# Optimization experiments

Hardware: AMD Instinct MI355X
Metric: run time of the kernel (lower is better)

## Reference

```python
import jax, jax.numpy as jnp
import numpy as np

N = 200000
IN_CH = 128
HIDDEN = [512, 512, 256]
NUM_TYPES = 10


def hetero_linear(x, types, W, b):
    # y[n] = x[n] @ W[types[n]] + b[types[n]]
    # Loop over the small fixed set of types (grouped GEMM as masked dense GEMMs).
    out = jnp.zeros((x.shape[0], W.shape[2]), dtype=x.dtype)
    for t in range(W.shape[0]):
        yt = x @ W[t] + b[t]
        out = out + jnp.where((types == t)[:, None], yt, jnp.zeros((), x.dtype))
    return out


def setup_inputs() -> dict:
    key = jax.random.key(0)
    ks = jax.random.split(key, 8)
    dims = [IN_CH] + HIDDEN
    inp = {
        "x": jax.random.normal(ks[0], (N, IN_CH), dtype=jnp.float32),
        "atom_types": jax.random.randint(ks[1], (N,), 0, NUM_TYPES, dtype=jnp.int32),
    }
    for i in range(3):
        fan_in = dims[i]
        scale = 1.0 / np.sqrt(fan_in)
        inp[f"W{i}"] = jax.random.normal(ks[2 + 2 * i], (NUM_TYPES, dims[i], dims[i + 1]), dtype=jnp.float32) * scale
        inp[f"b{i}"] = jax.random.normal(ks[3 + 2 * i], (NUM_TYPES, dims[i + 1]), dtype=jnp.float32) * scale
    return inp


def reference(x, atom_types, W0, b0, W1, b1, W2, b2):
    h = jax.nn.relu(hetero_linear(x, atom_types, W0, b0))
    h = jax.nn.relu(hetero_linear(h, atom_types, W1, b1))
    return hetero_linear(h, atom_types, W2, b2)
```

## Files before the change

kernel.cpp:

```cpp
#include <hip/hip_runtime.h>
#include <stdint.h>

typedef float  f32x4  __attribute__((ext_vector_type(4)));
typedef short  bf16x8 __attribute__((ext_vector_type(8)));

#define TYPES 10
#define D_IN  128
#define D_H1  512
#define D_H2  512
#define D_OUT 256

__device__ __forceinline__ unsigned short f2bf(float f) {
  union { float f; unsigned u; } v; v.f = f;
  unsigned u = v.u;
  return (unsigned short)((u + 0x7FFFu + ((u >> 16) & 1u)) >> 16);
}

__device__ __forceinline__ void async16(void* lds, const void* g) {
  __builtin_amdgcn_global_load_lds(
      (const __attribute__((address_space(1))) void*)g,
      (__attribute__((address_space(3))) void*)lds, 16, 0, 0);
}

__global__ void k_init(int* meta) {
  if (threadIdx.x < 48) meta[threadIdx.x] = 0;
}

__global__ void k_hist(const int* __restrict__ types, int n, int* __restrict__ meta) {
  __shared__ int lc[TYPES];
  if (threadIdx.x < TYPES) lc[threadIdx.x] = 0;
  __syncthreads();
  int i = blockIdx.x * 256 + threadIdx.x;
  if (i < n) atomicAdd(&lc[types[i]], 1);
  __syncthreads();
  if (threadIdx.x < TYPES && lc[threadIdx.x]) atomicAdd(&meta[threadIdx.x], lc[threadIdx.x]);
}

__global__ void k_scan(int* meta) {
  if (threadIdx.x == 0) {
    int off = 0;
    for (int t = 0; t < TYPES; ++t) {
      meta[16 + t] = off;
      off += ((meta[t] + 127) >> 7) << 7;
    }
    meta[26] = off;
  }
}

__global__ void k_scatter(const int* __restrict__ types, int n,
                          int* __restrict__ meta, int* __restrict__ perm) {
  __shared__ int lc[TYPES], lbase[TYPES];
  if (threadIdx.x < TYPES) lc[threadIdx.x] = 0;
  __syncthreads();
  int i = blockIdx.x * 256 + threadIdx.x;
  int t = 0, loc = 0;
  bool ok = i < n;
  if (ok) { t = types[i]; loc = atomicAdd(&lc[t], 1); }
  __syncthreads();
  if (threadIdx.x < TYPES) {
    int c = lc[threadIdx.x];
    lbase[threadIdx.x] = c ? atomicAdd(&meta[32 + threadIdx.x], c) : 0;
  }
  __syncthreads();
  if (ok) perm[meta[16 + t] + lbase[t] + loc] = i;
}

__global__ void k_gather(const float* __restrict__ x, const int* __restrict__ perm,
                         const int* __restrict__ meta, unsigned short* __restrict__ xs) {
  int p = blockIdx.x * 8 + (threadIdx.x >> 5);
  if (p >= meta[26]) return;
  int t = 0;
  while (p >= meta[17 + t]) t++;
  int e = (threadIdx.x & 31) * 4;
  unsigned short o0, o1, o2, o3;
  if (p - meta[16 + t] < meta[t]) {
    const float4 v = *(const float4*)(x + (size_t)perm[p] * D_IN + e);
    o0 = f2bf(v.x); o1 = f2bf(v.y); o2 = f2bf(v.z); o3 = f2bf(v.w);
  } else {
    o0 = o1 = o2 = o3 = 0;
  }
  *(ushort4*)(xs + (size_t)p * D_IN + e) = make_ushort4(o0, o1, o2, o3);
}

__global__ void k_wtrans(const float* __restrict__ W, unsigned short* __restrict__ Wt,
                         int K, int NOUT) {
  int t = blockIdx.y;
  int ntn = NOUT >> 6;
  int kb = blockIdx.x / ntn, nb = blockIdx.x % ntn;
  __shared__ unsigned short tile[64][65];
  const float* src = W + (size_t)t * K * NOUT + (size_t)(kb * 64) * NOUT + nb * 64;
  int c = threadIdx.x & 63;
  int r0 = threadIdx.x >> 6;
  #pragma unroll
  for (int i = 0; i < 16; ++i) {
    int r = r0 * 16 + i;
    tile[r][c] = f2bf(src[(size_t)r * NOUT + c]);
  }
  __syncthreads();
  unsigned short* dst = Wt + (size_t)t * NOUT * K + (size_t)(nb * 64) * K + kb * 64;
  #pragma unroll
  for (int i = 0; i < 16; ++i) {
    int nn = r0 * 16 + i;
    dst[(size_t)nn * K + c] = tile[c][nn];
  }
}

template <int K, int NOUT, bool RELU, bool FINAL>
__launch_bounds__(256)
__global__ void k_gemm(const unsigned short* __restrict__ A,
                       const unsigned short* __restrict__ Wt,
                       const float* __restrict__ bias,
                       unsigned short* __restrict__ H,
                       float* __restrict__ OUT,
                       const int* __restrict__ meta,
                       const int* __restrict__ perm) {
  __shared__ unsigned short As[128 * 32];
  __shared__ unsigned short Bs[128 * 32];
  int row0 = blockIdx.y * 128;
  if (row0 >= meta[26]) return;
  int t = 0;
  while (row0 >= meta[17 + t]) t++;
  int seg = meta[16 + t], cnt = meta[t];
  int tid = threadIdx.x, lane = tid & 63, wid = tid >> 6;
  int wr = (wid >> 1) * 64, wc = (wid & 1) * 64;
  int col0 = blockIdx.x * 128;
  const unsigned short* Ag = A + (size_t)row0 * K;
  const unsigned short* Bg = Wt + ((size_t)t * NOUT + col0) * K;

  f32x4 acc[4][4] = {};
  int r_ld = tid >> 2;
  int k_ld = (tid & 3) * 8;
  int ldsbase = (tid & ~63) * 8;

  constexpr int nK = K / 32;
  for (int kt = 0; kt < nK; ++kt) {
    __syncthreads();
    #pragma unroll
    for (int i = 0; i < 2; ++i) {
      int r = i * 64 + r_ld;
      async16(As + i * 2048 + ldsbase, Ag + (size_t)r * K + kt * 32 + k_ld);
      async16(Bs + i * 2048 + ldsbase, Bg + (size_t)r * K + kt * 32 + k_ld);
    }
    __syncthreads();

    int koff = (lane >> 4) * 8;
    int rA = lane & 15;
    bf16x8 a[4], b[4];
    #pragma unroll
    for (int m = 0; m < 4; ++m)
      a[m] = *(const bf16x8*)(As + (wr + m * 16 + rA) * 32 + koff);
    #pragma unroll
    for (int n = 0; n < 4; ++n)
      b[n] = *(const bf16x8*)(Bs + (wc + n * 16 + rA) * 32 + koff);
    #pragma unroll
    for (int m = 0; m < 4; ++m)
      #pragma unroll
      for (int n = 0; n < 4; ++n)
        acc[m][n] = __builtin_amdgcn_mfma_f32_16x16x32_bf16(a[m], b[n], acc[m][n], 0, 0, 0);
  }

  int cA = lane & 15, rE = (lane >> 4) * 4;
  #pragma unroll
  for (int n = 0; n < 4; ++n) {
    int col = col0 + wc + n * 16 + cA;
    float bv = bias[t * NOUT + col];
    #pragma unroll
    for (int m = 0; m < 4; ++m) {
      int rb = row0 + wr + m * 16 + rE;
      #pragma unroll
      for (int e = 0; e < 4; ++e) {
        float v = acc[m][n][e] + bv;
        if (RELU) v = fmaxf(v, 0.f);
        if (!FINAL) {
          H[(size_t)(rb + e) * NOUT + col] = f2bf(v);
        } else {
          int r = rb + e;
          if (r - seg < cnt) OUT[(size_t)perm[r] * NOUT + col] = v;
        }
      }
    }
  }
}

extern "C" void kernel_launch(void* const* d_in, const int* in_sizes, int n_in,
                              void* d_out, int out_size, void* d_ws, size_t ws_size,
                              hipStream_t stream) {
  const float* x     = (const float*)d_in[0];
  const int*   types = (const int*)d_in[1];
  const float* W0    = (const float*)d_in[2];
  const float* b0    = (const float*)d_in[3];
  const float* W1    = (const float*)d_in[4];
  const float* b1    = (const float*)d_in[5];
  const float* W2    = (const float*)d_in[6];
  const float* b2    = (const float*)d_in[7];
  float* out = (float*)d_out;
  int n = in_sizes[1];
  int RB = (n + 127) / 128 + TYPES;
  size_t NPAD = (size_t)RB * 128;

  char* ws = (char*)d_ws;
  int* meta = (int*)ws;
  int* perm = (int*)(ws + 1024);
  size_t off = 1024 + NPAD * 4;
  off = (off + 255) & ~(size_t)255;
  unsigned short* wt0 = (unsigned short*)(ws + off); off += (size_t)TYPES * D_H1 * D_IN * 2;
  unsigned short* wt1 = (unsigned short*)(ws + off); off += (size_t)TYPES * D_H2 * D_H1 * 2;
  unsigned short* wt2 = (unsigned short*)(ws + off); off += (size_t)TYPES * D_OUT * D_H2 * 2;
  off = (off + 255) & ~(size_t)255;
  unsigned short* B1 = (unsigned short*)(ws + off); off += NPAD * 512 * 2;
  unsigned short* B2 = (unsigned short*)(ws + off); off += NPAD * 512 * 2;

  int hb = (n + 255) / 256;
  k_init<<<1, 64, 0, stream>>>(meta);
  k_hist<<<hb, 256, 0, stream>>>(types, n, meta);
  k_scan<<<1, 64, 0, stream>>>(meta);
  k_scatter<<<hb, 256, 0, stream>>>(types, n, meta, perm);
  k_gather<<<RB * 16, 256, 0, stream>>>(x, perm, meta, B1);
  k_wtrans<<<dim3((D_IN / 64) * (D_H1 / 64), TYPES), 256, 0, stream>>>(W0, wt0, D_IN, D_H1);
  k_wtrans<<<dim3((D_H1 / 64) * (D_H2 / 64), TYPES), 256, 0, stream>>>(W1, wt1, D_H1, D_H2);
  k_wtrans<<<dim3((D_H2 / 64) * (D_OUT / 64), TYPES), 256, 0, stream>>>(W2, wt2, D_H2, D_OUT);

  k_gemm<D_IN, D_H1, true,  false><<<dim3(D_H1 / 128, RB), 256, 0, stream>>>(B1, wt0, b0, B2, nullptr, meta, perm);
  k_gemm<D_H1, D_H2, true,  false><<<dim3(D_H2 / 128, RB), 256, 0, stream>>>(B2, wt1, b1, B1, nullptr, meta, perm);
  k_gemm<D_H2, D_OUT, false, true ><<<dim3(D_OUT / 128, RB), 256, 0, stream>>>(B1, wt2, b2, nullptr, out, meta, perm);
}
```

Baseline: 528.0 us.

## Double-buffer GEMM K-loop with swizzled LDS, BK=64, and XCD-aware block remap

Reworks the grouped GEMM mainloop to use a 64-wide K tile, double-buffered in 64KB of LDS. The next tile's async global-to-LDS loads are issued before the current tile's MFMAs, so memory latency can overlap compute. An XOR swizzle on the 16-byte chunk index is meant to avoid LDS bank conflicts on the bf16x8 reads. Workgroup IDs are remapped so consecutive tiles land on the same XCD for better L2 reuse. The cost is lower occupancy from the larger LDS footprint.

```diff
diff --git a/kernel.cpp b/kernel.cpp
--- a/kernel.cpp
+++ b/kernel.cpp
@@ -114,49 +114,83 @@
                        float* __restrict__ OUT,
                        const int* __restrict__ meta,
                        const int* __restrict__ perm) {
-  __shared__ unsigned short As[128 * 32];
-  __shared__ unsigned short Bs[128 * 32];
-  int row0 = blockIdx.y * 128;
+  __shared__ char lds[65536];
+
+  int NXB = gridDim.x;
+  int nwg = NXB * (int)gridDim.y;
+  int raw = blockIdx.x + blockIdx.y * NXB;
+  int q = nwg >> 3, rr = nwg & 7;
+  int xcd = raw & 7, idx = raw >> 3;
+  int swz = (xcd < rr ? xcd * (q + 1) : rr * (q + 1) + (xcd - rr) * q) + idx;
+  int bx = swz % NXB, by = swz / NXB;
+
+  int row0 = by * 128;
   if (row0 >= meta[26]) return;
   int t = 0;
   while (row0 >= meta[17 + t]) t++;
   int seg = meta[16 + t], cnt = meta[t];
   int tid = threadIdx.x, lane = tid & 63, wid = tid >> 6;
   int wr = (wid >> 1) * 64, wc = (wid & 1) * 64;
-  int col0 = blockIdx.x * 128;
-  const unsigned short* Ag = A + (size_t)row0 * K;
-  const unsigned short* Bg = Wt + ((size_t)t * NOUT + col0) * K;
+  int col0 = bx * 128;
+  const char* Ag = (const char*)(A + (size_t)row0 * K);
+  const char* Bg = (const char*)(Wt + ((size_t)t * NOUT + col0) * K);
+
+  int srow = tid >> 3, sg = tid & 7;
+  const char* aSrc[4]; const char* bSrc[4]; int ldst[4];
+  #pragma unroll
+  for (int i = 0; i < 4; ++i) {
+    int r = i * 32 + srow;
+    int g = sg ^ (r & 7);
+    aSrc[i] = Ag + (size_t)r * (K * 2) + g * 16;
+    bSrc[i] = Bg + (size_t)r * (K * 2) + g * 16;
+    ldst[i] = i * 4096 + (tid >> 6) * 1024;
+  }
 
   f32x4 acc[4][4] = {};
-  int r_ld = tid >> 2;
-  int k_ld = (tid & 3) * 8;
-  int ldsbase = (tid & ~63) * 8;
-
-  constexpr int nK = K / 32;
+  int rA = lane & 15, qk = lane >> 4;
+
+  #pragma unroll
+  for (int i = 0; i < 4; ++i) {
+    async16(lds + ldst[i],         aSrc[i]);
+    async16(lds + 16384 + ldst[i], bSrc[i]);
+  }
+  __syncthreads();
+
+  constexpr int nK = K / 64;
   for (int kt = 0; kt < nK; ++kt) {
+    int cur = kt & 1;
+    if (kt + 1 < nK) {
+      char* nb_ = lds + (cur ^ 1) * 32768;
+      #pragma unroll
+      for (int i = 0; i < 4; ++i) {
+        async16(nb_ + ldst[i],         aSrc[i] + (size_t)(kt + 1) * 128);
+        async16(nb_ + 16384 + ldst[i], bSrc[i] + (size_t)(kt + 1) * 128);
+      }
+    }
+    const char* Ab = lds + cur * 32768;
+    const char* Bb = Ab + 16384;
+    #pragma unroll
+    for (int kk = 0; kk < 2; ++kk) {
+      bf16x8 a[4], b[4];
+      #pragma unroll
+      for (int m = 0; m < 4; ++m) {
+        int row = wr + m * 16 + rA;
+        int off = (row * 128 + kk * 64 + qk * 16) ^ ((rA & 7) << 4);
+        a[m] = *(const bf16x8*)(Ab + off);
+      }
+      #pragma unroll
+      for (int n = 0; n < 4; ++n) {
+        int row = wc + n * 16 + rA;
+        int off = (row * 128 + kk * 64 + qk * 16) ^ ((rA & 7) << 4);
+        b[n] = *(const bf16x8*)(Bb + off);
+      }
+      #pragma unroll
+      for (int m = 0; m < 4; ++m)
+        #pragma unroll
+        for (int n = 0; n < 4; ++n)
+          acc[m][n] = __builtin_amdgcn_mfma_f32_16x16x32_bf16(a[m], b[n], acc[m][n], 0, 0, 0);
+    }
     __syncthreads();
-    #pragma unroll
-    for (int i = 0; i < 2; ++i) {
-      int r = i * 64 + r_ld;
-      async16(As + i * 2048 + ldsbase, Ag + (size_t)r * K + kt * 32 + k_ld);
-      async16(Bs + i * 2048 + ldsbase, Bg + (size_t)r * K + kt * 32 + k_ld);
-    }
-    __syncthreads();
-
-    int koff = (lane >> 4) * 8;
-    int rA = lane & 15;
-    bf16x8 a[4], b[4];
-    #pragma unroll
-    for (int m = 0; m < 4; ++m)
-      a[m] = *(const bf16x8*)(As + (wr + m * 16 + rA) * 32 + koff);
-    #pragma unroll
-    for (int n = 0; n < 4; ++n)
-      b[n] = *(const bf16x8*)(Bs + (wc + n * 16 + rA) * 32 + koff);
-    #pragma unroll
-    for (int m = 0; m < 4; ++m)
-      #pragma unroll
-      for (int n = 0; n < 4; ++n)
-        acc[m][n] = __builtin_amdgcn_mfma_f32_16x16x32_bf16(a[m], b[n], acc[m][n], 0, 0, 0);
   }
 
   int cA = lane & 15, rE = (lane >> 4) * 4;
```

After: 598.6 us. +13.4%, slower.

## Rewrite grouped GEMM as 256x256 tile, double-buffered, swizzled-LDS pipelined kernel

Applied to the files above, without the earlier changes.

Grows the GEMM block tile from 128x128 to 256x256 with 8 waves and a K step of 64. Global-to-LDS async loads are double-buffered and interleaved across four sub-phases, with XOR-swizzled LDS addressing and explicit waitcnt/barrier/setprio scheduling. Blocks are remapped across XCDs for cache locality. Segment padding per type rises to 256 rows to match the new tile. The aim is to hide load latency and raise MFMA utilisation, at the cost of 128 KB LDS per block, more register pressure, and more padded rows per type.

```diff
diff --git a/kernel.cpp b/kernel.cpp
--- a/kernel.cpp
+++ b/kernel.cpp
@@ -41,7 +41,7 @@
     int off = 0;
     for (int t = 0; t < TYPES; ++t) {
       meta[16 + t] = off;
-      off += ((meta[t] + 127) >> 7) << 7;
+      off += ((meta[t] + 255) >> 8) << 8;
     }
     meta[26] = off;
   }
@@ -106,7 +106,7 @@
 }
 
 template <int K, int NOUT, bool RELU, bool FINAL>
-__launch_bounds__(256)
+__launch_bounds__(512, 2)
 __global__ void k_gemm(const unsigned short* __restrict__ A,
                        const unsigned short* __restrict__ Wt,
                        const float* __restrict__ bias,
@@ -114,62 +114,113 @@
                        float* __restrict__ OUT,
                        const int* __restrict__ meta,
                        const int* __restrict__ perm) {
-  __shared__ unsigned short As[128 * 32];
-  __shared__ unsigned short Bs[128 * 32];
-  int row0 = blockIdx.y * 128;
+  constexpr int nKT = K / 64;
+  __shared__ char lds[131072];
+
+  int NXB = gridDim.x;
+  int nwg = NXB * (int)gridDim.y;
+  int raw = blockIdx.x + blockIdx.y * NXB;
+  int q = nwg >> 3, rr = nwg & 7;
+  int xcd = raw & 7, idx = raw >> 3;
+  int swz = (xcd < rr ? xcd * (q + 1) : rr * (q + 1) + (xcd - rr) * q) + idx;
+  int bx = swz % NXB, by = swz / NXB;
+
+  int row0 = by * 256;
   if (row0 >= meta[26]) return;
   int t = 0;
   while (row0 >= meta[17 + t]) t++;
   int seg = meta[16 + t], cnt = meta[t];
   int tid = threadIdx.x, lane = tid & 63, wid = tid >> 6;
-  int wr = (wid >> 1) * 64, wc = (wid & 1) * 64;
-  int col0 = blockIdx.x * 128;
-  const unsigned short* Ag = A + (size_t)row0 * K;
-  const unsigned short* Bg = Wt + ((size_t)t * NOUT + col0) * K;
-
-  f32x4 acc[4][4] = {};
-  int r_ld = tid >> 2;
-  int k_ld = (tid & 3) * 8;
-  int ldsbase = (tid & ~63) * 8;
-
-  constexpr int nK = K / 32;
-  for (int kt = 0; kt < nK; ++kt) {
-    __syncthreads();
+  int wr = (wid >> 2) * 128, wc = (wid & 3) * 64;
+  int col0 = bx * 256;
+  const char* Ag = (const char*)(A + (size_t)row0 * K);
+  const char* Bg = (const char*)(Wt + ((size_t)t * NOUT + col0) * K);
+
+  int gsrc = ((tid & 7) ^ ((tid >> 3) & 7)) * 16;
+  const char* aS = Ag + (size_t)(tid >> 3) * (2 * K) + gsrc;
+  const char* bS = Bg + (size_t)(((tid >> 3) & 31) + ((tid >> 3) >> 5) * 64) * (2 * K) + gsrc;
+
+  auto stage = [&](int kt, int sub) {
+    if (kt >= nKT) return;
+    int h = sub & 1, du = kt & 1;
+    char* dst = lds + ((sub < 2) ? 0 : 65536) + (du * 2 + h) * 16384 + wid * 1024;
+    const char* src = (sub < 2 ? aS + (size_t)(h * 64) * (2 * K)
+                               : bS + (size_t)(h * 32) * (2 * K)) + (size_t)kt * 128;
+    async16(dst,        src);
+    async16(dst + 8192, src + (size_t)128 * (2 * K));
+  };
+
+  f32x4 acc[8][4] = {};
+  int rA = lane & 15, qoff = (lane >> 4) * 16, xr = (lane & 7) << 4;
+  int lrA = (wid >> 2) * 64;
+  int clB = (wid & 3) * 32;
+
+  stage(0, 2); stage(0, 1); stage(0, 0); stage(0, 3); stage(1, 2); stage(1, 1);
+  asm volatile("s_waitcnt vmcnt(4)" ::: "memory");
+  __builtin_amdgcn_s_barrier();
+
+  for (int g = 0; g < nKT; ++g) {
+    int d = g & 1;
+    const char* Ad = lds + d * 32768;
+    const char* Bd = lds + 65536 + d * 32768;
     #pragma unroll
-    for (int i = 0; i < 2; ++i) {
-      int r = i * 64 + r_ld;
-      async16(As + i * 2048 + ldsbase, Ag + (size_t)r * K + kt * 32 + k_ld);
-      async16(Bs + i * 2048 + ldsbase, Bg + (size_t)r * K + kt * 32 + k_ld);
+    for (int rel = 0; rel < 4; ++rel) {
+      constexpr int MH[4] = {0, 1, 1, 0};
+      constexpr int NH[4] = {0, 0, 1, 1};
+      const int mh = MH[rel], nh = NH[rel];
+      const char* Au = Ad + mh * 16384;
+      const char* Bu = Bd + nh * 16384;
+      bf16x8 a[4][2], b[2][2];
+      #pragma unroll
+      for (int m = 0; m < 4; ++m) {
+        int lr = lrA + m * 16 + rA;
+        #pragma unroll
+        for (int kk = 0; kk < 2; ++kk)
+          a[m][kk] = *(const bf16x8*)(Au + ((lr * 128 + kk * 64 + qoff) ^ xr));
+      }
+      #pragma unroll
+      for (int nn = 0; nn < 2; ++nn) {
+        int cl = clB + nn * 16 + rA;
+        #pragma unroll
+        for (int kk = 0; kk < 2; ++kk)
+          b[nn][kk] = *(const bf16x8*)(Bu + ((cl * 128 + kk * 64 + qoff) ^ xr));
+      }
+      if      (rel == 0) stage(g + 1, 0);
+      else if (rel == 1) stage(g + 1, 3);
+      else if (rel == 2) stage(g + 2, 2);
+      else               stage(g + 2, 1);
+      __builtin_amdgcn_s_barrier();
+      asm volatile("s_waitcnt lgkmcnt(0)" ::: "memory");
+      __builtin_amdgcn_sched_barrier(0);
+      __builtin_amdgcn_s_setprio(1);
+      #pragma unroll
+      for (int kk = 0; kk < 2; ++kk)
+        #pragma unroll
+        for (int m = 0; m < 4; ++m)
+          #pragma unroll
+          for (int nn = 0; nn < 2; ++nn)
+            acc[mh * 4 + m][nh * 2 + nn] = __builtin_amdgcn_mfma_f32_16x16x32_bf16(
+                a[m][kk], b[nn][kk], acc[mh * 4 + m][nh * 2 + nn], 0, 0, 0);
+      __builtin_amdgcn_s_setprio(0);
+      if (rel == 3 && g + 1 < nKT) {
+        if (g + 2 < nKT) asm volatile("s_waitcnt vmcnt(4)" ::: "memory");
+        else             asm volatile("s_waitcnt vmcnt(0)" ::: "memory");
+      }
+      __builtin_amdgcn_s_barrier();
     }
-    __syncthreads();
-
-    int koff = (lane >> 4) * 8;
-    int rA = lane & 15;
-    bf16x8 a[4], b[4];
-    #pragma unroll
-    for (int m = 0; m < 4; ++m)
-      a[m] = *(const bf16x8*)(As + (wr + m * 16 + rA) * 32 + koff);
-    #pragma unroll
-    for (int n = 0; n < 4; ++n)
-      b[n] = *(const bf16x8*)(Bs + (wc + n * 16 + rA) * 32 + koff);
-    #pragma unroll
-    for (int m = 0; m < 4; ++m)
-      #pragma unroll
-      for (int n = 0; n < 4; ++n)
-        acc[m][n] = __builtin_amdgcn_mfma_f32_16x16x32_bf16(a[m], b[n], acc[m][n], 0, 0, 0);
   }
 
   int cA = lane & 15, rE = (lane >> 4) * 4;
   #pragma unroll
-  for (int n = 0; n < 4; ++n) {
-    int col = col0 + wc + n * 16 + cA;
+  for (int ni = 0; ni < 4; ++ni) {
+    int col = col0 + wc + ni * 16 + cA;
     float bv = bias[t * NOUT + col];
     #pragma unroll
-    for (int m = 0; m < 4; ++m) {
-      int rb = row0 + wr + m * 16 + rE;
+    for (int mi = 0; mi < 8; ++mi) {
+      int rb = row0 + wr + mi * 16 + rE;
       #pragma unroll
       for (int e = 0; e < 4; ++e) {
-        float v = acc[m][n][e] + bv;
+        float v = acc[mi][ni][e] + bv;
         if (RELU) v = fmaxf(v, 0.f);
         if (!FINAL) {
           H[(size_t)(rb + e) * NOUT + col] = f2bf(v);
@@ -195,8 +246,8 @@
   const float* b2    = (const float*)d_in[7];
   float* out = (float*)d_out;
   int n = in_sizes[1];
-  int RB = (n + 127) / 128 + TYPES;
-  size_t NPAD = (size_t)RB * 128;
+  int RB = (n + 255) / 256 + TYPES;
+  size_t NPAD = (size_t)RB * 256;
 
   char* ws = (char*)d_ws;
   int* meta = (int*)ws;
@@ -215,12 +266,12 @@
   k_hist<<<hb, 256, 0, stream>>>(types, n, meta);
   k_scan<<<1, 64, 0, stream>>>(meta);
   k_scatter<<<hb, 256, 0, stream>>>(types, n, meta, perm);
-  k_gather<<<RB * 16, 256, 0, stream>>>(x, perm, meta, B1);
+  k_gather<<<RB * 32, 256, 0, stream>>>(x, perm, meta, B1);
   k_wtrans<<<dim3((D_IN / 64) * (D_H1 / 64), TYPES), 256, 0, stream>>>(W0, wt0, D_IN, D_H1);
   k_wtrans<<<dim3((D_H1 / 64) * (D_H2 / 64), TYPES), 256, 0, stream>>>(W1, wt1, D_H1, D_H2);
   k_wtrans<<<dim3((D_H2 / 64) * (D_OUT / 64), TYPES), 256, 0, stream>>>(W2, wt2, D_H2, D_OUT);
 
-  k_gemm<D_IN, D_H1, true,  false><<<dim3(D_H1 / 128, RB), 256, 0, stream>>>(B1, wt0, b0, B2, nullptr, meta, perm);
-  k_gemm<D_H1, D_H2, true,  false><<<dim3(D_H2 / 128, RB), 256, 0, stream>>>(B2, wt1, b1, B1, nullptr, meta, perm);
-  k_gemm<D_H2, D_OUT, false, true ><<<dim3(D_OUT / 128, RB), 256, 0, stream>>>(B1, wt2, b2, nullptr, out, meta, perm);
-}
+  k_gemm<D_IN, D_H1, true,  false><<<dim3(D_H1 / 256, RB), 512, 0, stream>>>(B1, wt0, b0, B2, nullptr, meta, perm);
+  k_gemm<D_H1, D_H2, true,  false><<<dim3(D_H2 / 256, RB), 512, 0, stream>>>(B2, wt1, b1, B1, nullptr, meta, perm);
+  k_gemm<D_H2, D_OUT, false, true ><<<dim3(D_OUT / 256, RB), 512, 0, stream>>>(B1, wt2, b2, nullptr, out, meta, perm);
+}
```

Result: slower. 542.4 us (+2.7%).

## Fuse gather and all three MLP layers into one LDS-resident kernel

Applied to the files above, without the earlier changes.

Replaces the gather kernel and the three separate grouped GEMM launches with a single kernel. Each 128-row block of sorted rows keeps its activations in a 160KB LDS tile across all layers and streams weight tiles double-buffered with swizzled layouts. It also merges the three weight-transpose launches into one and remaps block indices across XCDs. This removes the global round-trips of the bf16 hidden activations and several launches. The cost is heavy LDS use, which limits occupancy, and barrier-heavy inner loops.

```diff
diff --git a/kernel.cpp b/kernel.cpp
--- a/kernel.cpp
+++ b/kernel.cpp
@@ -65,28 +65,17 @@
   if (ok) perm[meta[16 + t] + lbase[t] + loc] = i;
 }
 
-__global__ void k_gather(const float* __restrict__ x, const int* __restrict__ perm,
-                         const int* __restrict__ meta, unsigned short* __restrict__ xs) {
-  int p = blockIdx.x * 8 + (threadIdx.x >> 5);
-  if (p >= meta[26]) return;
-  int t = 0;
-  while (p >= meta[17 + t]) t++;
-  int e = (threadIdx.x & 31) * 4;
-  unsigned short o0, o1, o2, o3;
-  if (p - meta[16 + t] < meta[t]) {
-    const float4 v = *(const float4*)(x + (size_t)perm[p] * D_IN + e);
-    o0 = f2bf(v.x); o1 = f2bf(v.y); o2 = f2bf(v.z); o3 = f2bf(v.w);
-  } else {
-    o0 = o1 = o2 = o3 = 0;
-  }
-  *(ushort4*)(xs + (size_t)p * D_IN + e) = make_ushort4(o0, o1, o2, o3);
-}
-
-__global__ void k_wtrans(const float* __restrict__ W, unsigned short* __restrict__ Wt,
-                         int K, int NOUT) {
-  int t = blockIdx.y;
+__global__ void k_wtrans_all(const float* __restrict__ W0a, const float* __restrict__ W1a,
+                             const float* __restrict__ W2a,
+                             unsigned short* __restrict__ wt0, unsigned short* __restrict__ wt1,
+                             unsigned short* __restrict__ wt2) {
+  int b = blockIdx.x;
+  const float* W; unsigned short* Wt; int K, NOUT, t, local;
+  if (b < 160)      { W = W0a; Wt = wt0; K = 128; NOUT = 512; t = b / 16; local = b % 16; }
+  else if (b < 800) { b -= 160; W = W1a; Wt = wt1; K = 512; NOUT = 512; t = b / 64; local = b % 64; }
+  else              { b -= 800; W = W2a; Wt = wt2; K = 512; NOUT = 256; t = b / 32; local = b % 32; }
   int ntn = NOUT >> 6;
-  int kb = blockIdx.x / ntn, nb = blockIdx.x % ntn;
+  int kb = local / ntn, nb = local % ntn;
   __shared__ unsigned short tile[64][65];
   const float* src = W + (size_t)t * K * NOUT + (size_t)(kb * 64) * NOUT + nb * 64;
   int c = threadIdx.x & 63;
@@ -105,78 +94,188 @@
   }
 }
 
-template <int K, int NOUT, bool RELU, bool FINAL>
-__launch_bounds__(256)
-__global__ void k_gemm(const unsigned short* __restrict__ A,
-                       const unsigned short* __restrict__ Wt,
-                       const float* __restrict__ bias,
-                       unsigned short* __restrict__ H,
-                       float* __restrict__ OUT,
-                       const int* __restrict__ meta,
-                       const int* __restrict__ perm) {
-  __shared__ unsigned short As[128 * 32];
-  __shared__ unsigned short Bs[128 * 32];
-  int row0 = blockIdx.y * 128;
+__device__ __forceinline__ void stageW(char* lds, int tid, int wid,
+                                       const unsigned short* __restrict__ Wt,
+                                       int NOUTl, int Kl, int t, int nb, int kt, int slot) {
+  const char* base = (const char*)(Wt + ((size_t)t * NOUTl + nb * 128) * Kl);
+  int lr = tid >> 3;
+  int g = ((tid & 7) ^ (lr & 7)) * 16;
+  const char* s0 = base + (size_t)lr * (Kl * 2) + (size_t)kt * 128 + g;
+  char* dst = lds + 131072 + slot * 16384 + wid * 1024;
+  async16(dst, s0);
+  async16(dst + 8192, s0 + (size_t)64 * (Kl * 2));
+}
+
+template <int KT, int NB>
+__device__ __forceinline__ void run_layer(char* lds, const unsigned short* __restrict__ Wt,
+                                          int Kl, int NOUTl, int t, int tid, int wid, int lane,
+                                          f32x4 (&acc)[4][8]) {
+  int rA = lane & 15, qk = (lane >> 4) * 16;
+  int wr = (wid >> 2) * 64, wcg = wid & 3;
+  bf16x8 a[4][2], b[2][2];
+  for (int kt = 0; kt < KT; ++kt) {
+    #pragma unroll
+    for (int nb = 0; nb < NB; ++nb) {
+      __builtin_amdgcn_sched_barrier(0);
+      const int slot = nb & 1;
+      if (nb == 0) {
+        #pragma unroll
+        for (int m = 0; m < 4; ++m) {
+          int r = wr + m * 16 + rA;
+          #pragma unroll
+          for (int kk = 0; kk < 2; ++kk)
+            a[m][kk] = *(const bf16x8*)(lds + r * 1024 +
+                         ((kt * 128 + kk * 64 + qk) ^ ((r & 7) << 4)));
+        }
+      }
+      #pragma unroll
+      for (int n = 0; n < 2; ++n) {
+        int cl = wcg * 32 + n * 16 + rA;
+        #pragma unroll
+        for (int kk = 0; kk < 2; ++kk)
+          b[n][kk] = *(const bf16x8*)(lds + 131072 + slot * 16384 + cl * 128 +
+                       ((kk * 64 + qk) ^ ((cl & 7) << 4)));
+      }
+      if (nb + 1 < NB)      stageW(lds, tid, wid, Wt, NOUTl, Kl, t, nb + 1, kt, (nb + 1) & 1);
+      else if (kt + 1 < KT) stageW(lds, tid, wid, Wt, NOUTl, Kl, t, 0, kt + 1, 0);
+      __builtin_amdgcn_s_barrier();
+      asm volatile("s_waitcnt lgkmcnt(0)" ::: "memory");
+      __builtin_amdgcn_sched_barrier(0);
+      __builtin_amdgcn_s_setprio(1);
+      #pragma unroll
+      for (int kk = 0; kk < 2; ++kk)
+        #pragma unroll
+        for (int m = 0; m < 4; ++m)
+          #pragma unroll
+          for (int n = 0; n < 2; ++n)
+            acc[m][nb * 2 + n] = __builtin_amdgcn_mfma_f32_16x16x32_bf16(
+                a[m][kk], b[n][kk], acc[m][nb * 2 + n], 0, 0, 0);
+      __builtin_amdgcn_s_setprio(0);
+      asm volatile("s_waitcnt vmcnt(0)" ::: "memory");
+      __builtin_amdgcn_s_barrier();
+    }
+  }
+}
+
+template <int CF, bool RELU>
+__device__ __forceinline__ void writeback_h(char* lds, const float* __restrict__ bias_,
+                                            int NOUTl, int t, int wid, int lane,
+                                            f32x4 (&acc)[4][8]) {
+  int cA = lane & 15, rE = (lane >> 4) * 4;
+  int wr = (wid >> 2) * 64, wcg = wid & 3;
+  #pragma unroll
+  for (int cf = 0; cf < CF; ++cf) {
+    int col = (cf >> 1) * 128 + wcg * 32 + (cf & 1) * 16 + cA;
+    float bv = bias_[t * NOUTl + col];
+    #pragma unroll
+    for (int m = 0; m < 4; ++m)
+      #pragma unroll
+      for (int e = 0; e < 4; ++e) {
+        int row = wr + m * 16 + rE + e;
+        float v = acc[m][cf][e] + bv;
+        if (RELU) v = fmaxf(v, 0.f);
+        *(unsigned short*)(lds + row * 1024 + ((col * 2) ^ ((row & 7) << 4))) = f2bf(v);
+      }
+  }
+}
+
+__launch_bounds__(512, 2)
+__global__ void k_fused(const float* __restrict__ x,
+                        const unsigned short* __restrict__ wt0, const float* __restrict__ b0,
+                        const unsigned short* __restrict__ wt1, const float* __restrict__ b1,
+                        const unsigned short* __restrict__ wt2, const float* __restrict__ b2,
+                        float* __restrict__ out,
+                        const int* __restrict__ meta, const int* __restrict__ perm) {
+  __shared__ char lds[163840];
+
+  int nwg = gridDim.x, raw = blockIdx.x;
+  int q = nwg >> 3, rr = nwg & 7;
+  int xcd = raw & 7, idx = raw >> 3;
+  int swz = (xcd < rr ? xcd * (q + 1) : rr * (q + 1) + (xcd - rr) * q) + idx;
+
+  int row0 = swz * 128;
   if (row0 >= meta[26]) return;
   int t = 0;
   while (row0 >= meta[17 + t]) t++;
   int seg = meta[16 + t], cnt = meta[t];
   int tid = threadIdx.x, lane = tid & 63, wid = tid >> 6;
-  int wr = (wid >> 1) * 64, wc = (wid & 1) * 64;
-  int col0 = blockIdx.x * 128;
-  const unsigned short* Ag = A + (size_t)row0 * K;
-  const unsigned short* Bg = Wt + ((size_t)t * NOUT + col0) * K;
-
-  f32x4 acc[4][4] = {};
-  int r_ld = tid >> 2;
-  int k_ld = (tid & 3) * 8;
-  int ldsbase = (tid & ~63) * 8;
-
-  constexpr int nK = K / 32;
-  for (int kt = 0; kt < nK; ++kt) {
-    __syncthreads();
-    #pragma unroll
-    for (int i = 0; i < 2; ++i) {
-      int r = i * 64 + r_ld;
-      async16(As + i * 2048 + ldsbase, Ag + (size_t)r * K + kt * 32 + k_ld);
-      async16(Bs + i * 2048 + ldsbase, Bg + (size_t)r * K + kt * 32 + k_ld);
-    }
-    __syncthreads();
-
-    int koff = (lane >> 4) * 8;
-    int rA = lane & 15;
-    bf16x8 a[4], b[4];
-    #pragma unroll
-    for (int m = 0; m < 4; ++m)
-      a[m] = *(const bf16x8*)(As + (wr + m * 16 + rA) * 32 + koff);
-    #pragma unroll
-    for (int n = 0; n < 4; ++n)
-      b[n] = *(const bf16x8*)(Bs + (wc + n * 16 + rA) * 32 + koff);
-    #pragma unroll
-    for (int m = 0; m < 4; ++m)
-      #pragma unroll
-      for (int n = 0; n < 4; ++n)
-        acc[m][n] = __builtin_amdgcn_mfma_f32_16x16x32_bf16(a[m], b[n], acc[m][n], 0, 0, 0);
-  }
-
-  int cA = lane & 15, rE = (lane >> 4) * 4;
-  #pragma unroll
-  for (int n = 0; n < 4; ++n) {
-    int col = col0 + wc + n * 16 + cA;
-    float bv = bias[t * NOUT + col];
-    #pragma unroll
-    for (int m = 0; m < 4; ++m) {
-      int rb = row0 + wr + m * 16 + rE;
-      #pragma unroll
-      for (int e = 0; e < 4; ++e) {
-        float v = acc[m][n][e] + bv;
-        if (RELU) v = fmaxf(v, 0.f);
-        if (!FINAL) {
-          H[(size_t)(rb + e) * NOUT + col] = f2bf(v);
-        } else {
-          int r = rb + e;
-          if (r - seg < cnt) OUT[(size_t)perm[r] * NOUT + col] = v;
+
+  stageW(lds, tid, wid, wt0, D_H1, D_IN, t, 0, 0, 0);
+
+  {
+    int grow = tid >> 2, gch = tid & 3;
+    int p = row0 + grow;
+    bool ok = (unsigned)(p - seg) < (unsigned)cnt;
+    int sw = (grow & 7) << 4;
+    const float* sp = ok ? x + (size_t)perm[p] * D_IN + gch * 32 : nullptr;
+    #pragma unroll
+    for (int j = 0; j < 4; ++j) {
+      bf16x8 v = {0, 0, 0, 0, 0, 0, 0, 0};
+      if (ok) {
+        float4 f0 = *(const float4*)(sp + j * 8);
+        float4 f1 = *(const float4*)(sp + j * 8 + 4);
+        v[0] = (short)f2bf(f0.x); v[1] = (short)f2bf(f0.y);
+        v[2] = (short)f2bf(f0.z); v[3] = (short)f2bf(f0.w);
+        v[4] = (short)f2bf(f1.x); v[5] = (short)f2bf(f1.y);
+        v[6] = (short)f2bf(f1.z); v[7] = (short)f2bf(f1.w);
+      }
+      *(bf16x8*)(lds + grow * 1024 + ((((gch * 4 + j) * 16)) ^ sw)) = v;
+    }
+  }
+  __syncthreads();
+
+  f32x4 acc[4][8];
+  #pragma unroll
+  for (int m = 0; m < 4; ++m)
+    #pragma unroll
+    for (int cf = 0; cf < 8; ++cf) acc[m][cf] = (f32x4){0.f, 0.f, 0.f, 0.f};
+
+  run_layer<2, 4>(lds, wt0, D_IN, D_H1, t, tid, wid, lane, acc);
+  stageW(lds, tid, wid, wt1, D_H2, D_H1, t, 0, 0, 0);
+  writeback_h<8, true>(lds, b0, D_H1, t, wid, lane, acc);
+  __syncthreads();
+  #pragma unroll
+  for (int m = 0; m < 4; ++m)
+    #pragma unroll
+    for (int cf = 0; cf < 8; ++cf) acc[m][cf] = (f32x4){0.f, 0.f, 0.f, 0.f};
+
+  run_layer<8, 4>(lds, wt1, D_H1, D_H2, t, tid, wid, lane, acc);
+  stageW(lds, tid, wid, wt2, D_OUT, D_H2, t, 0, 0, 0);
+  writeback_h<8, true>(lds, b1, D_H2, t, wid, lane, acc);
+  __syncthreads();
+  #pragma unroll
+  for (int m = 0; m < 4; ++m)
+    #pragma unroll
+    for (int cf = 0; cf < 8; ++cf) acc[m][cf] = (f32x4){0.f, 0.f, 0.f, 0.f};
+
+  run_layer<8, 2>(lds, wt2, D_H2, D_OUT, t, tid, wid, lane, acc);
+
+  {
+    int cA = lane & 15, rE = (lane >> 4) * 4;
+    int wr = (wid >> 2) * 64, wcg = wid & 3;
+    #pragma unroll
+    for (int cf = 0; cf < 4; ++cf) {
+      int col = (cf >> 1) * 128 + wcg * 32 + (cf & 1) * 16 + cA;
+      float bv = b2[t * D_OUT + col];
+      #pragma unroll
+      for (int m = 0; m < 4; ++m)
+        #pragma unroll
+        for (int e = 0; e < 4; ++e) {
+          int row = wr + m * 16 + rE + e;
+          *(float*)(lds + row * 1024 + ((col * 4) ^ ((row & 7) << 4))) = acc[m][cf][e] + bv;
         }
+    }
+    __builtin_amdgcn_s_barrier();
+    int grow = tid >> 2, gch = tid & 3;
+    int p = row0 + grow;
+    bool ok = (unsigned)(p - seg) < (unsigned)cnt;
+    if (ok) {
+      float* op = out + (size_t)perm[p] * D_OUT + gch * 64;
+      int sw = (grow & 7) << 4;
+      #pragma unroll
+      for (int j = 0; j < 16; ++j) {
+        float4 v = *(const float4*)(lds + grow * 1024 + ((((gch * 16 + j) * 16)) ^ sw));
+        *(float4*)(op + j * 4) = v;
       }
     }
   }
@@ -206,21 +305,13 @@
   unsigned short* wt0 = (unsigned short*)(ws + off); off += (size_t)TYPES * D_H1 * D_IN * 2;
   unsigned short* wt1 = (unsigned short*)(ws + off); off += (size_t)TYPES * D_H2 * D_H1 * 2;
   unsigned short* wt2 = (unsigned short*)(ws + off); off += (size_t)TYPES * D_OUT * D_H2 * 2;
-  off = (off + 255) & ~(size_t)255;
-  unsigned short* B1 = (unsigned short*)(ws + off); off += NPAD * 512 * 2;
-  unsigned short* B2 = (unsigned short*)(ws + off); off += NPAD * 512 * 2;
 
   int hb = (n + 255) / 256;
   k_init<<<1, 64, 0, stream>>>(meta);
   k_hist<<<hb, 256, 0, stream>>>(types, n, meta);
   k_scan<<<1, 64, 0, stream>>>(meta);
   k_scatter<<<hb, 256, 0, stream>>>(types, n, meta, perm);
-  k_gather<<<RB * 16, 256, 0, stream>>>(x, perm, meta, B1);
-  k_wtrans<<<dim3((D_IN / 64) * (D_H1 / 64), TYPES), 256, 0, stream>>>(W0, wt0, D_IN, D_H1);
-  k_wtrans<<<dim3((D_H1 / 64) * (D_H2 / 64), TYPES), 256, 0, stream>>>(W1, wt1, D_H1, D_H2);
-  k_wtrans<<<dim3((D_H2 / 64) * (D_OUT / 64), TYPES), 256, 0, stream>>>(W2, wt2, D_H2, D_OUT);
-
-  k_gemm<D_IN, D_H1, true,  false><<<dim3(D_H1 / 128, RB), 256, 0, stream>>>(B1, wt0, b0, B2, nullptr, meta, perm);
-  k_gemm<D_H1, D_H2, true,  false><<<dim3(D_H2 / 128, RB), 256, 0, stream>>>(B2, wt1, b1, B1, nullptr, meta, perm);
-  k_gemm<D_H2, D_OUT, false, true ><<<dim3(D_OUT / 128, RB), 256, 0, stream>>>(B1, wt2, b2, nullptr, out, meta, perm);
-}
+  k_wtrans_all<<<1120, 256, 0, stream>>>(W0, W1, W2, wt0, wt1, wt2);
+
+  k_fused<<<RB, 512, 0, stream>>>(x, wt0, b0, wt1, b1, wt2, b2, out, meta, perm);
+}
```

Result: slower. 550.5 us (+4.3%).
